# Kernel optimization log

Measured on AMD Instinct MI355X. Metric: run time of the kernel, lower is better.

## Reference

```python
import jax, jax.numpy as jnp
import numpy as np

B, H, W = 32, 512, 512

def _sample(img, sx, sy):
    """Bilinear sample img [C,H,W] at source coords sx,sy [H,W]; zeros padding (align_corners=True pixel coords)."""
    C, Hh, Ww = img.shape
    x0 = jnp.floor(sx); y0 = jnp.floor(sy)
    wx = sx - x0; wy = sy - y0
    def gat(xf, yf):
        xi = jnp.clip(xf, 0, Ww - 1).astype(jnp.int32)
        yi = jnp.clip(yf, 0, Hh - 1).astype(jnp.int32)
        valid = ((xf >= 0) & (xf <= Ww - 1) & (yf >= 0) & (yf <= Hh - 1)).astype(img.dtype)
        return img[:, yi, xi] * valid
    return (gat(x0, y0) * (1 - wx) * (1 - wy) + gat(x0 + 1, y0) * wx * (1 - wy)
            + gat(x0, y0 + 1) * (1 - wx) * wy + gat(x0 + 1, y0 + 1) * wx * wy)

def _grid(Hh, Ww, dtype):
    ys, xs = jnp.meshgrid(jnp.arange(Hh, dtype=dtype), jnp.arange(Ww, dtype=dtype), indexing='ij')
    return xs, ys

def _rotate_one(img, angle_deg):
    C, Hh, Ww = img.shape
    th = angle_deg * (jnp.pi / 180.0)
    c, s = jnp.cos(th), jnp.sin(th)
    cx, cy = (Ww - 1) / 2.0, (Hh - 1) / 2.0
    xs, ys = _grid(Hh, Ww, img.dtype)
    dx, dy = xs - cx, ys - cy
    return _sample(img, c * dx + s * dy + cx, -s * dx + c * dy + cy)

def _affine_one(img, tx, ty, sc):
    C, Hh, Ww = img.shape
    cx, cy = (Ww - 1) / 2.0, (Hh - 1) / 2.0
    xs, ys = _grid(Hh, Ww, img.dtype)
    return _sample(img, (xs - cx - tx) / sc + cx, (ys - cy - ty) / sc + cy)

def _rgb_to_hsv(img):
    r, g, b = img[:, 0], img[:, 1], img[:, 2]
    maxc = jnp.maximum(jnp.maximum(r, g), b)
    minc = jnp.minimum(jnp.minimum(r, g), b)
    delta = maxc - minc
    eps = 1e-8
    s = delta / (maxc + eps)
    dd = delta + eps
    rc, gc, bc = (maxc - r) / dd, (maxc - g) / dd, (maxc - b) / dd
    h = jnp.where(maxc == r, bc - gc, jnp.where(maxc == g, 2.0 + rc - bc, 4.0 + gc - rc))
    return (h / 6.0) % 1.0, s, maxc

def _hsv_to_rgb(h, s, v):
    i = jnp.floor(h * 6.0)
    f = h * 6.0 - i
    p, q, t = v * (1 - s), v * (1 - f * s), v * (1 - (1 - f) * s)
    i = i.astype(jnp.int32) % 6
    conds = [i == k for k in range(6)]
    r = jnp.select(conds, [v, q, p, p, t, v])
    g = jnp.select(conds, [t, v, v, q, p, p])
    b = jnp.select(conds, [p, p, t, v, v, q])
    return jnp.stack([r, g, b], axis=1)

def _color_jitter(img, bf, cf, sf, hf):
    bf, cf, sf = (x[:, None, None, None] for x in (bf, cf, sf))
    img = jnp.clip(img * bf, 0.0, 1.0)
    gray = (0.299 * img[:, 0] + 0.587 * img[:, 1] + 0.114 * img[:, 2])[:, None]
    mean = gray.mean(axis=(2, 3), keepdims=True)
    img = jnp.clip(cf * img + (1 - cf) * mean, 0.0, 1.0)
    gray = (0.299 * img[:, 0] + 0.587 * img[:, 1] + 0.114 * img[:, 2])[:, None]
    img = jnp.clip(sf * img + (1 - sf) * gray, 0.0, 1.0)
    h, s, v = _rgb_to_hsv(img)
    h = (h + hf[:, None, None]) % 1.0
    return jnp.clip(_hsv_to_rgb(h, s, v), 0.0, 1.0)

def _forward(imgs, masks, hflip_mask, vflip_mask, angles, translate, scale, brightness, contrast, saturation, hue):
    hm = (hflip_mask > 0)[:, None, None, None]
    vm = (vflip_mask > 0)[:, None, None, None]
    imgs = jnp.where(hm, imgs[..., ::-1], imgs)
    masks = jnp.where(hm, masks[..., ::-1], masks)
    imgs = jnp.where(vm, imgs[..., ::-1, :], imgs)
    masks = jnp.where(vm, masks[..., ::-1, :], masks)
    rot = jax.vmap(_rotate_one)
    imgs = rot(imgs, angles)
    masks = rot(masks, angles)
    tx = translate[:, 0] * W
    ty = translate[:, 1] * H
    aff = jax.vmap(_affine_one)
    imgs = aff(imgs, tx, ty, scale)
    masks = aff(masks, tx, ty, scale)
    imgs = _color_jitter(imgs, brightness, contrast, saturation, hue)
    return imgs, masks

def setup_inputs():
    key = jax.random.key(0)
    ks = jax.random.split(key, 11)
    return {
        "imgs": jax.random.uniform(ks[0], (B, 3, H, W), jnp.float32),
        "masks": (jax.random.uniform(ks[1], (B, 1, H, W)) > 0.5).astype(jnp.float32),
        "hflip_mask": jax.random.randint(ks[2], (B,), 0, 2, jnp.int32),
        "vflip_mask": jax.random.randint(ks[3], (B,), 0, 2, jnp.int32),
        "angles": (jax.random.uniform(ks[4], (B,)) - 0.5) * 180.0,
        "translate": (jax.random.uniform(ks[5], (B, 2)) - 0.5) * 0.2,
        "scale": 0.9 + jax.random.uniform(ks[6], (B,)) * 0.2,
        "brightness": 0.8 + jax.random.uniform(ks[7], (B,)) * 0.4,
        "contrast": 0.8 + jax.random.uniform(ks[8], (B,)) * 0.4,
        "saturation": 0.8 + jax.random.uniform(ks[9], (B,)) * 0.4,
        "hue": (jax.random.uniform(ks[10], (B,)) - 0.5) * 0.2,
    }

def reference(imgs, masks, hflip_mask, vflip_mask, angles, translate, scale, brightness, contrast, saturation, hue):
    return _forward(imgs, masks, hflip_mask, vflip_mask, angles, translate, scale, brightness, contrast, saturation, hue)
```

## Files before the change

### kernel.cpp

```cpp
#include <hip/hip_runtime.h>
#include <hip/hip_fp16.h>
#include <math.h>

#define Wd 512
#define Hd 512
#define Bd 32
#define PLANE (Hd * Wd)

#define WIN 48
#define WSTR 49

#define RPW 40
#define RPH 22

__device__ __forceinline__ float clip01(float x) { return fminf(fmaxf(x, 0.f), 1.f); }

__device__ __forceinline__ unsigned pack2h(float a, float b) {
    __half2 h = __floats2half2_rn(a, b);
    return *(unsigned*)&h;
}
__device__ __forceinline__ float2 unp2h(unsigned u) {
    return __half22float2(*(__half2*)&u);
}

__global__ __launch_bounds__(256) void k_rotate(const float* __restrict__ imgs,
                                                const float* __restrict__ masks,
                                                const int* __restrict__ hflip,
                                                const int* __restrict__ vflip,
                                                const float* __restrict__ angles,
                                                uint2* __restrict__ rot)
{
    __shared__ uint2 cells[WIN * WSTR];

    const int hw = blockIdx.x;
    const int lt = (hw & 7) * 1024 + (hw >> 3);
    const int b   = lt >> 8;
    const int t   = lt & 255;
    const int bx  = (t & 15) * 32;
    const int by  = (t >> 4) * 32;

    const int tx = threadIdx.x, ty = threadIdx.y;
    const int tid = ty * 32 + tx;

    const float cx = (Wd - 1) * 0.5f, cy = (Hd - 1) * 0.5f;
    const float th = angles[b] * 0.017453292519943295f;
    const float c = cosf(th), s = sinf(th);
    const bool hf = hflip[b] > 0, vf = vflip[b] > 0;

    const float xs0 = (float)bx - cx, xs1 = (float)(bx + 31) - cx;
    const float ys0 = (float)by - cy, ys1 = (float)(by + 31) - cy;
    float a0 = c * xs0 + s * ys0 + cx, a1 = c * xs1 + s * ys0 + cx;
    float a2 = c * xs0 + s * ys1 + cx, a3 = c * xs1 + s * ys1 + cx;
    float b0 = -s * xs0 + c * ys0 + cy, b1 = -s * xs1 + c * ys0 + cy;
    float b2 = -s * xs0 + c * ys1 + cy, b3 = -s * xs1 + c * ys1 + cy;
    float mnx = fminf(fminf(a0, a1), fminf(a2, a3));
    float mxx = fmaxf(fmaxf(a0, a1), fmaxf(a2, a3));
    float mny = fminf(fminf(b0, b1), fminf(b2, b3));
    float mxy = fmaxf(fmaxf(b0, b1), fmaxf(b2, b3));
    const int ox0 = (int)floorf(hf ? (511.f - mxx) : mnx) - 1;
    const int oy0 = (int)floorf(vf ? (511.f - mxy) : mny) - 1;

    const float* ib = imgs + (size_t)b * 3 * PLANE;
    const float* mb = masks + (size_t)b * PLANE;

    #pragma unroll
    for (int it = 0; it < 9; ++it) {
        int slot = tid + it * 256;
        int row = slot / WIN;
        int col = slot - row * WIN;
        int gi = min(max(oy0 + row, 0), Hd - 1) * Wd + min(max(ox0 + col, 0), Wd - 1);
        float r = ib[gi];
        float g = ib[gi + PLANE];
        float bl = ib[gi + 2 * PLANE];
        float m = mb[gi];
        cells[row * WSTR + col] = make_uint2(pack2h(r, g), pack2h(bl, m));
    }
    __syncthreads();

    #pragma unroll
    for (int k = 0; k < 4; ++k) {
        const int x = bx + tx, y = by + ty + k * 8;
        float dx = (float)x - cx, dy = (float)y - cy;
        float sx = c * dx + s * dy + cx;
        float sy = -s * dx + c * dy + cy;
        if (hf) sx = 511.f - sx;
        if (vf) sy = 511.f - sy;

        float sxl = sx - (float)ox0, syl = sy - (float)oy0;
        float x0f = floorf(sxl), y0f = floorf(syl);
        float wx = sxl - x0f, wy = syl - y0f;
        int xi = min(max((int)x0f, 0), WIN - 2);
        int yi = min(max((int)y0f, 0), WIN - 2);

        float fx0 = (float)ox0 + x0f, fy0 = (float)oy0 + y0f;
        float vx0 = (fx0 >= 0.f && fx0 <= 511.f) ? 1.f : 0.f;
        float vx1 = (fx0 >= -1.f && fx0 <= 510.f) ? 1.f : 0.f;
        float vy0 = (fy0 >= 0.f && fy0 <= 511.f) ? 1.f : 0.f;
        float vy1 = (fy0 >= -1.f && fy0 <= 510.f) ? 1.f : 0.f;
        float w00 = (1.f - wx) * (1.f - wy) * vx0 * vy0;
        float w10 = wx * (1.f - wy) * vx1 * vy0;
        float w01 = (1.f - wx) * wy * vx0 * vy1;
        float w11 = wx * wy * vx1 * vy1;

        int base = yi * WSTR + xi;
        uint2 c00 = cells[base],        c10 = cells[base + 1];
        uint2 c01 = cells[base + WSTR], c11 = cells[base + WSTR + 1];

        float2 rg00 = unp2h(c00.x), bm00 = unp2h(c00.y);
        float2 rg10 = unp2h(c10.x), bm10 = unp2h(c10.y);
        float2 rg01 = unp2h(c01.x), bm01 = unp2h(c01.y);
        float2 rg11 = unp2h(c11.x), bm11 = unp2h(c11.y);

        float r  = w00 * rg00.x + w10 * rg10.x + w01 * rg01.x + w11 * rg11.x;
        float g  = w00 * rg00.y + w10 * rg10.y + w01 * rg01.y + w11 * rg11.y;
        float bl = w00 * bm00.x + w10 * bm10.x + w01 * bm01.x + w11 * bm11.x;
        float m  = w00 * bm00.y + w10 * bm10.y + w01 * bm01.y + w11 * bm11.y;

        rot[(size_t)b * PLANE + (size_t)y * Wd + x] =
            make_uint2(pack2h(r, g), pack2h(bl, m));
    }
}

__global__ __launch_bounds__(256) void k_affine(const ushort4* __restrict__ rot,
                                                const float* __restrict__ translate,
                                                const float* __restrict__ scale,
                                                const float* __restrict__ brightness,
                                                unsigned short* __restrict__ pre,
                                                float* __restrict__ omasks,
                                                float* __restrict__ partials)
{
    __shared__ float4 tile[RPH * RPW];

    const int tx2 = threadIdx.x;
    const int ty  = threadIdx.y;
    const int tid = ty * 16 + tx2;
    const int bx = blockIdx.x * 32, by = blockIdx.y * 16;
    const int b = blockIdx.z;

    const float cx = (Wd - 1) * 0.5f, cy = (Hd - 1) * 0.5f;
    const float txf = translate[2 * b] * (float)Wd;
    const float tyf = translate[2 * b + 1] * (float)Hd;
    const float sc = scale[b];
    const float bf = brightness[b];

    float ax0 = ((float)bx - cx - txf) / sc + cx;
    float ax1 = ((float)(bx + 31) - cx - txf) / sc + cx;
    float ay0 = ((float)by - cy - tyf) / sc + cy;
    float ay1 = ((float)(by + 15) - cy - tyf) / sc + cy;
    const int rx0 = (int)floorf(fminf(ax0, ax1)) - 1;
    const int ry0 = (int)floorf(fminf(ay0, ay1)) - 1;

    const ushort4* srcp = rot + (size_t)b * PLANE;
    const bool fastp = (rx0 >= 0) && (ry0 >= 0) &&
                       (rx0 + RPW <= Wd) && (ry0 + RPH <= Hd);

    if (fastp) {
        for (int idx = tid; idx < RPH * RPW; idx += 256) {
            int row = idx / RPW;
            int col = idx - row * RPW;
            ushort4 h = srcp[(ry0 + row) * Wd + rx0 + col];
            tile[idx] = make_float4(__half2float(__ushort_as_half(h.x)),
                                    __half2float(__ushort_as_half(h.y)),
                                    __half2float(__ushort_as_half(h.z)),
                                    __half2float(__ushort_as_half(h.w)));
        }
    } else {
        for (int idx = tid; idx < RPH * RPW; idx += 256) {
            int row = idx / RPW;
            int col = idx - row * RPW;
            int gy = ry0 + row, gx = rx0 + col;
            float4 v = make_float4(0.f, 0.f, 0.f, 0.f);
            if ((unsigned)gy < (unsigned)Hd && (unsigned)gx < (unsigned)Wd) {
                ushort4 h = srcp[gy * Wd + gx];
                v = make_float4(__half2float(__ushort_as_half(h.x)),
                                __half2float(__ushort_as_half(h.y)),
                                __half2float(__ushort_as_half(h.z)),
                                __half2float(__ushort_as_half(h.w)));
            }
            tile[idx] = v;
        }
    }
    __syncthreads();

    float grays = 0.f;
    float rr[2], gg[2], bb[2], mm[2];
    #pragma unroll
    for (int k = 0; k < 2; ++k) {
        int x = bx + 2 * tx2 + k, y = by + ty;
        float sx = ((float)x - cx - txf) / sc + cx;
        float sy = ((float)y - cy - tyf) / sc + cy;
        float sxl = sx - (float)rx0, syl = sy - (float)ry0;
        float x0f = floorf(sxl), y0f = floorf(syl);
        float wx = sxl - x0f, wy = syl - y0f;
        int xi = min(max((int)x0f, 0), RPW - 2);
        int yi = min(max((int)y0f, 0), RPH - 2);
        float w00 = (1.f - wx) * (1.f - wy);
        float w10 = wx * (1.f - wy);
        float w01 = (1.f - wx) * wy;
        float w11 = wx * wy;
        int base = yi * RPW + xi;
        float4 v00 = tile[base], v10 = tile[base + 1];
        float4 v01 = tile[base + RPW], v11 = tile[base + RPW + 1];
        float r  = w00 * v00.x + w10 * v10.x + w01 * v01.x + w11 * v11.x;
        float g  = w00 * v00.y + w10 * v10.y + w01 * v01.y + w11 * v11.y;
        float b2 = w00 * v00.z + w10 * v10.z + w01 * v01.z + w11 * v11.z;
        float m  = w00 * v00.w + w10 * v10.w + w01 * v01.w + w11 * v11.w;
        r = clip01(r * bf);
        g = clip01(g * bf);
        b2 = clip01(b2 * bf);
        rr[k] = r; gg[k] = g; bb[k] = b2; mm[k] = m;
        grays += 0.299f * r + 0.587f * g + 0.114f * b2;
    }
    {
        size_t pix = (size_t)(by + ty) * Wd + bx + 2 * tx2;
        unsigned short* pb = pre + (size_t)b * 3 * PLANE;
        *(unsigned*)(pb + pix)             = pack2h(rr[0], rr[1]);
        *(unsigned*)(pb + PLANE + pix)     = pack2h(gg[0], gg[1]);
        *(unsigned*)(pb + 2 * PLANE + pix) = pack2h(bb[0], bb[1]);
        *(float2*)(omasks + (size_t)b * PLANE + pix) = make_float2(mm[0], mm[1]);
    }

    __syncthreads();
    float* sred = (float*)tile;
    sred[tid] = grays;
    __syncthreads();
    for (int off = 128; off > 0; off >>= 1) {
        if (tid < off) sred[tid] += sred[tid + off];
        __syncthreads();
    }
    if (tid == 0)
        partials[(size_t)b * 512 + blockIdx.y * 16 + blockIdx.x] = sred[0];
}

__global__ __launch_bounds__(256) void k_mean(const float* __restrict__ partials,
                                              float* __restrict__ means)
{
    int b = blockIdx.x;
    int t = threadIdx.x;
    float s = partials[(size_t)b * 512 + t] + partials[(size_t)b * 512 + t + 256];
    __shared__ float sr[256];
    sr[t] = s;
    __syncthreads();
    for (int off = 128; off > 0; off >>= 1) {
        if (t < off) sr[t] += sr[t + off];
        __syncthreads();
    }
    if (t == 0) means[b] = sr[0] * (1.f / (float)PLANE);
}

__device__ __forceinline__ void jit1(float& r, float& g, float& bl,
                                     float mean, float cf, float sf, float hsh)
{
    r  = clip01(cf * r + (1.f - cf) * mean);
    g  = clip01(cf * g + (1.f - cf) * mean);
    bl = clip01(cf * bl + (1.f - cf) * mean);

    float gray = 0.299f * r + 0.587f * g + 0.114f * bl;
    r  = clip01(sf * r + (1.f - sf) * gray);
    g  = clip01(sf * g + (1.f - sf) * gray);
    bl = clip01(sf * bl + (1.f - sf) * gray);

    float maxc = fmaxf(fmaxf(r, g), bl);
    float minc = fminf(fminf(r, g), bl);
    float delta = maxc - minc;
    float sgm = delta / (maxc + 1e-8f);
    float dd = delta + 1e-8f;
    float rc = (maxc - r) / dd;
    float gc = (maxc - g) / dd;
    float bc = (maxc - bl) / dd;
    float h6 = (maxc == r) ? (bc - gc) : ((maxc == g) ? (2.f + rc - bc) : (4.f + gc - rc));
    float h = h6 * (1.f / 6.f);
    h = h - floorf(h);
    h = h + hsh;
    h = h - floorf(h);

    float hi = floorf(h * 6.f);
    float f = h * 6.f - hi;
    float v = maxc;
    float p = v * (1.f - sgm);
    float q = v * (1.f - f * sgm);
    float t = v * (1.f - (1.f - f) * sgm);
    int i = ((int)hi) % 6;
    if (i < 0) i += 6;
    float ro, go, bo;
    switch (i) {
        case 0: ro = v; go = t; bo = p; break;
        case 1: ro = q; go = v; bo = p; break;
        case 2: ro = p; go = v; bo = t; break;
        case 3: ro = p; go = q; bo = v; break;
        case 4: ro = t; go = p; bo = v; break;
        default: ro = v; go = p; bo = q; break;
    }
    r = clip01(ro); g = clip01(go); bl = clip01(bo);
}

__global__ __launch_bounds__(256) void k_jitter(const unsigned short* __restrict__ pre,
                                                const float* __restrict__ means,
                                                const float* __restrict__ contrast,
                                                const float* __restrict__ saturation,
                                                const float* __restrict__ hue,
                                                float* __restrict__ oimgs)
{
    int b = blockIdx.y;
    size_t i4 = (size_t)blockIdx.x * 256 + threadIdx.x;
    const unsigned short* pb = pre + (size_t)b * 3 * PLANE;

    uint2 ur = *(const uint2*)(pb + i4 * 4);
    uint2 ug = *(const uint2*)(pb + PLANE + i4 * 4);
    uint2 ub = *(const uint2*)(pb + 2 * PLANE + i4 * 4);

    float2 r01 = unp2h(ur.x), r23 = unp2h(ur.y);
    float2 g01 = unp2h(ug.x), g23 = unp2h(ug.y);
    float2 b01 = unp2h(ub.x), b23 = unp2h(ub.y);

    float4 R  = make_float4(r01.x, r01.y, r23.x, r23.y);
    float4 G  = make_float4(g01.x, g01.y, g23.x, g23.y);
    float4 Bv = make_float4(b01.x, b01.y, b23.x, b23.y);

    float mean = means[b];
    float cf = contrast[b], sf = saturation[b], hsh = hue[b];

    jit1(R.x, G.x, Bv.x, mean, cf, sf, hsh);
    jit1(R.y, G.y, Bv.y, mean, cf, sf, hsh);
    jit1(R.z, G.z, Bv.z, mean, cf, sf, hsh);
    jit1(R.w, G.w, Bv.w, mean, cf, sf, hsh);

    size_t po = (size_t)b * 3 * PLANE + i4 * 4;
    *(float4*)(oimgs + po)             = R;
    *(float4*)(oimgs + po + PLANE)     = G;
    *(float4*)(oimgs + po + 2 * PLANE) = Bv;
}

extern "C" void kernel_launch(void* const* d_in, const int* in_sizes, int n_in,
                              void* d_out, int out_size, void* d_ws, size_t ws_size,
                              hipStream_t stream)
{
    const float* imgs       = (const float*)d_in[0];
    const float* masks      = (const float*)d_in[1];
    const int*   hflip      = (const int*)d_in[2];
    const int*   vflip      = (const int*)d_in[3];
    const float* angles     = (const float*)d_in[4];
    const float* translate  = (const float*)d_in[5];
    const float* scale      = (const float*)d_in[6];
    const float* brightness = (const float*)d_in[7];
    const float* contrast   = (const float*)d_in[8];
    const float* saturation = (const float*)d_in[9];
    const float* hue        = (const float*)d_in[10];

    float* oimgs  = (float*)d_out;
    float* omasks = oimgs + (size_t)Bd * 3 * PLANE;

    uint2* rot          = (uint2*)d_ws;
    unsigned short* pre = (unsigned short*)(rot + (size_t)Bd * PLANE);
    float* partials     = (float*)(pre + (size_t)3 * Bd * PLANE);
    float* means        = partials + (size_t)Bd * 512;

    dim3 blk1(32, 8);
    dim3 grd1(Bd * 16 * 16);
    k_rotate<<<grd1, blk1, 0, stream>>>(imgs, masks, hflip, vflip, angles, rot);

    dim3 blk2(16, 16);
    dim3 grd2(Wd / 32, Hd / 16, Bd);
    k_affine<<<grd2, blk2, 0, stream>>>((const ushort4*)rot, translate, scale, brightness,
                                        pre, omasks, partials);

    k_mean<<<Bd, 256, 0, stream>>>(partials, means);

    dim3 grd3(PLANE / 4 / 256, Bd);
    k_jitter<<<grd3, 256, 0, stream>>>(pre, means, contrast, saturation, hue, oimgs);
}
```

Measured before the change: 128.7 us.

## Vectorize halo loads, enlarge affine tiles to 32x32, keep half-precision tiles, remap blocks

The rotate kernel now aligns its halo window to even columns and loads two pixels per thread with float2 reads, writing 16-byte packed cells to shared memory. The affine kernel grows its output tile from 32x16 to 32x32 over a 40x40 window, which cuts halo overhead per output pixel. It also keeps the tile in packed half precision instead of converting to float4, which shrinks shared memory. Out-of-range samples are now zeroed through per-corner validity weights instead of a separate slow path. Blocks are remapped with a swizzled 1D grid, likely to spread them across XCDs, and the partial-sum count drops to 256 per image. The risks are more per-pixel arithmetic and possible shared-memory bank conflicts from the new strides.

```diff
diff --git a/kernel.cpp b/kernel.cpp
--- a/kernel.cpp
+++ b/kernel.cpp
@@ -8,10 +8,12 @@
 #define PLANE (Hd * Wd)
 
 #define WIN 48
-#define WSTR 49
-
-#define RPW 40
-#define RPH 22
+#define WSTR 50
+#define NPR1 (WIN * (WIN / 2))
+
+#define AWIN 40
+#define ASTR 42
+#define NPR2 (AWIN * (AWIN / 2))
 
 __device__ __forceinline__ float clip01(float x) { return fminf(fmaxf(x, 0.f), 1.f); }
 
@@ -57,23 +59,32 @@
     float mxx = fmaxf(fmaxf(a0, a1), fmaxf(a2, a3));
     float mny = fminf(fminf(b0, b1), fminf(b2, b3));
     float mxy = fmaxf(fmaxf(b0, b1), fmaxf(b2, b3));
-    const int ox0 = (int)floorf(hf ? (511.f - mxx) : mnx) - 1;
+    const int ox0 = ((int)floorf(hf ? (511.f - mxx) : mnx) - 1) & ~1;
     const int oy0 = (int)floorf(vf ? (511.f - mxy) : mny) - 1;
 
     const float* ib = imgs + (size_t)b * 3 * PLANE;
     const float* mb = masks + (size_t)b * PLANE;
 
     #pragma unroll
-    for (int it = 0; it < 9; ++it) {
+    for (int it = 0; it < 5; ++it) {
         int slot = tid + it * 256;
-        int row = slot / WIN;
-        int col = slot - row * WIN;
-        int gi = min(max(oy0 + row, 0), Hd - 1) * Wd + min(max(ox0 + col, 0), Wd - 1);
-        float r = ib[gi];
-        float g = ib[gi + PLANE];
-        float bl = ib[gi + 2 * PLANE];
-        float m = mb[gi];
-        cells[row * WSTR + col] = make_uint2(pack2h(r, g), pack2h(bl, m));
+        if (it < 4 || slot < NPR1) {
+            int row = slot / (WIN / 2);
+            int pc  = slot - row * (WIN / 2);
+            int gy = min(max(oy0 + row, 0), Hd - 1);
+            int gx = min(max(ox0 + 2 * pc, 0), Wd - 2) & ~1;
+            int gi = gy * Wd + gx;
+            float2 r2 = *(const float2*)(ib + gi);
+            float2 g2 = *(const float2*)(ib + gi + PLANE);
+            float2 b2v = *(const float2*)(ib + gi + 2 * PLANE);
+            float2 m2 = *(const float2*)(mb + gi);
+            uint4 w;
+            w.x = pack2h(r2.x, g2.x);
+            w.y = pack2h(b2v.x, m2.x);
+            w.z = pack2h(r2.y, g2.y);
+            w.w = pack2h(b2v.y, m2.y);
+            *(uint4*)&cells[row * WSTR + 2 * pc] = w;
+        }
     }
     __syncthreads();
 
@@ -121,7 +132,7 @@
     }
 }
 
-__global__ __launch_bounds__(256) void k_affine(const ushort4* __restrict__ rot,
+__global__ __launch_bounds__(256) void k_affine(const uint2* __restrict__ rot,
                                                 const float* __restrict__ translate,
                                                 const float* __restrict__ scale,
                                                 const float* __restrict__ brightness,
@@ -129,13 +140,18 @@
                                                 float* __restrict__ omasks,
                                                 float* __restrict__ partials)
 {
-    __shared__ float4 tile[RPH * RPW];
+    __shared__ uint2 tile[AWIN * ASTR];
+
+    const int hw = blockIdx.x;
+    const int lt = (hw & 7) * 1024 + (hw >> 3);
+    const int b   = lt >> 8;
+    const int t   = lt & 255;
+    const int bx  = (t & 15) * 32;
+    const int by  = (t >> 4) * 32;
 
     const int tx2 = threadIdx.x;
     const int ty  = threadIdx.y;
     const int tid = ty * 16 + tx2;
-    const int bx = blockIdx.x * 32, by = blockIdx.y * 16;
-    const int b = blockIdx.z;
 
     const float cx = (Wd - 1) * 0.5f, cy = (Hd - 1) * 0.5f;
     const float txf = translate[2 * b] * (float)Wd;
@@ -146,73 +162,72 @@
     float ax0 = ((float)bx - cx - txf) / sc + cx;
     float ax1 = ((float)(bx + 31) - cx - txf) / sc + cx;
     float ay0 = ((float)by - cy - tyf) / sc + cy;
-    float ay1 = ((float)(by + 15) - cy - tyf) / sc + cy;
-    const int rx0 = (int)floorf(fminf(ax0, ax1)) - 1;
+    float ay1 = ((float)(by + 31) - cy - tyf) / sc + cy;
+    const int rx0 = (((int)floorf(fminf(ax0, ax1)) - 1) & ~1);
     const int ry0 = (int)floorf(fminf(ay0, ay1)) - 1;
 
-    const ushort4* srcp = rot + (size_t)b * PLANE;
-    const bool fastp = (rx0 >= 0) && (ry0 >= 0) &&
-                       (rx0 + RPW <= Wd) && (ry0 + RPH <= Hd);
-
-    if (fastp) {
-        for (int idx = tid; idx < RPH * RPW; idx += 256) {
-            int row = idx / RPW;
-            int col = idx - row * RPW;
-            ushort4 h = srcp[(ry0 + row) * Wd + rx0 + col];
-            tile[idx] = make_float4(__half2float(__ushort_as_half(h.x)),
-                                    __half2float(__ushort_as_half(h.y)),
-                                    __half2float(__ushort_as_half(h.z)),
-                                    __half2float(__ushort_as_half(h.w)));
+    const uint2* sb = rot + (size_t)b * PLANE;
+
+    #pragma unroll
+    for (int it = 0; it < 4; ++it) {
+        int slot = tid + it * 256;
+        if (it < 3 || slot < NPR2) {
+            int row = slot / (AWIN / 2);
+            int pc  = slot - row * (AWIN / 2);
+            int gy = min(max(ry0 + row, 0), Hd - 1);
+            int gx = min(max(rx0 + 2 * pc, 0), Wd - 2) & ~1;
+            uint4 v = *(const uint4*)(sb + gy * Wd + gx);
+            *(uint4*)&tile[row * ASTR + 2 * pc] = v;
         }
-    } else {
-        for (int idx = tid; idx < RPH * RPW; idx += 256) {
-            int row = idx / RPW;
-            int col = idx - row * RPW;
-            int gy = ry0 + row, gx = rx0 + col;
-            float4 v = make_float4(0.f, 0.f, 0.f, 0.f);
-            if ((unsigned)gy < (unsigned)Hd && (unsigned)gx < (unsigned)Wd) {
-                ushort4 h = srcp[gy * Wd + gx];
-                v = make_float4(__half2float(__ushort_as_half(h.x)),
-                                __half2float(__ushort_as_half(h.y)),
-                                __half2float(__ushort_as_half(h.z)),
-                                __half2float(__ushort_as_half(h.w)));
-            }
-            tile[idx] = v;
+    }
+    __syncthreads();
+
+    float grays = 0.f;
+    #pragma unroll
+    for (int j = 0; j < 2; ++j) {
+        float rr[2], gg[2], bb[2], mm[2];
+        const int y = by + ty + 16 * j;
+        #pragma unroll
+        for (int k = 0; k < 2; ++k) {
+            int x = bx + 2 * tx2 + k;
+            float sx = ((float)x - cx - txf) / sc + cx;
+            float sy = ((float)y - cy - tyf) / sc + cy;
+            float sxl = sx - (float)rx0, syl = sy - (float)ry0;
+            float x0f = floorf(sxl), y0f = floorf(syl);
+            float wx = sxl - x0f, wy = syl - y0f;
+            int xi = min(max((int)x0f, 0), AWIN - 2);
+            int yi = min(max((int)y0f, 0), AWIN - 2);
+
+            float fx0 = (float)rx0 + x0f, fy0 = (float)ry0 + y0f;
+            float vx0 = (fx0 >= 0.f && fx0 <= 511.f) ? 1.f : 0.f;
+            float vx1 = (fx0 >= -1.f && fx0 <= 510.f) ? 1.f : 0.f;
+            float vy0 = (fy0 >= 0.f && fy0 <= 511.f) ? 1.f : 0.f;
+            float vy1 = (fy0 >= -1.f && fy0 <= 510.f) ? 1.f : 0.f;
+            float w00 = (1.f - wx) * (1.f - wy) * vx0 * vy0;
+            float w10 = wx * (1.f - wy) * vx1 * vy0;
+            float w01 = (1.f - wx) * wy * vx0 * vy1;
+            float w11 = wx * wy * vx1 * vy1;
+
+            int base = yi * ASTR + xi;
+            uint2 c00 = tile[base],        c10 = tile[base + 1];
+            uint2 c01 = tile[base + ASTR], c11 = tile[base + ASTR + 1];
+            float2 rg00 = unp2h(c00.x), bm00 = unp2h(c00.y);
+            float2 rg10 = unp2h(c10.x), bm10 = unp2h(c10.y);
+            float2 rg01 = unp2h(c01.x), bm01 = unp2h(c01.y);
+            float2 rg11 = unp2h(c11.x), bm11 = unp2h(c11.y);
+
+            float r  = w00 * rg00.x + w10 * rg10.x + w01 * rg01.x + w11 * rg11.x;
+            float g  = w00 * rg00.y + w10 * rg10.y + w01 * rg01.y + w11 * rg11.y;
+            float b2 = w00 * bm00.x + w10 * bm10.x + w01 * bm01.x + w11 * bm11.x;
+            float m  = w00 * bm00.y + w10 * bm10.y + w01 * bm01.y + w11 * bm11.y;
+
+            r = clip01(r * bf);
+            g = clip01(g * bf);
+            b2 = clip01(b2 * bf);
+            rr[k] = r; gg[k] = g; bb[k] = b2; mm[k] = m;
+            grays += 0.299f * r + 0.587f * g + 0.114f * b2;
         }
-    }
-    __syncthreads();
-
-    float grays = 0.f;
-    float rr[2], gg[2], bb[2], mm[2];
-    #pragma unroll
-    for (int k = 0; k < 2; ++k) {
-        int x = bx + 2 * tx2 + k, y = by + ty;
-        float sx = ((float)x - cx - txf) / sc + cx;
-        float sy = ((float)y - cy - tyf) / sc + cy;
-        float sxl = sx - (float)rx0, syl = sy - (float)ry0;
-        float x0f = floorf(sxl), y0f = floorf(syl);
-        float wx = sxl - x0f, wy = syl - y0f;
-        int xi = min(max((int)x0f, 0), RPW - 2);
-        int yi = min(max((int)y0f, 0), RPH - 2);
-        float w00 = (1.f - wx) * (1.f - wy);
-        float w10 = wx * (1.f - wy);
-        float w01 = (1.f - wx) * wy;
-        float w11 = wx * wy;
-        int base = yi * RPW + xi;
-        float4 v00 = tile[base], v10 = tile[base + 1];
-        float4 v01 = tile[base + RPW], v11 = tile[base + RPW + 1];
-        float r  = w00 * v00.x + w10 * v10.x + w01 * v01.x + w11 * v11.x;
-        float g  = w00 * v00.y + w10 * v10.y + w01 * v01.y + w11 * v11.y;
-        float b2 = w00 * v00.z + w10 * v10.z + w01 * v01.z + w11 * v11.z;
-        float m  = w00 * v00.w + w10 * v10.w + w01 * v01.w + w11 * v11.w;
-        r = clip01(r * bf);
-        g = clip01(g * bf);
-        b2 = clip01(b2 * bf);
-        rr[k] = r; gg[k] = g; bb[k] = b2; mm[k] = m;
-        grays += 0.299f * r + 0.587f * g + 0.114f * b2;
-    }
-    {
-        size_t pix = (size_t)(by + ty) * Wd + bx + 2 * tx2;
+        size_t pix = (size_t)y * Wd + bx + 2 * tx2;
         unsigned short* pb = pre + (size_t)b * 3 * PLANE;
         *(unsigned*)(pb + pix)             = pack2h(rr[0], rr[1]);
         *(unsigned*)(pb + PLANE + pix)     = pack2h(gg[0], gg[1]);
@@ -229,7 +244,7 @@
         __syncthreads();
     }
     if (tid == 0)
-        partials[(size_t)b * 512 + blockIdx.y * 16 + blockIdx.x] = sred[0];
+        partials[(size_t)b * 256 + t] = sred[0];
 }
 
 __global__ __launch_bounds__(256) void k_mean(const float* __restrict__ partials,
@@ -237,7 +252,7 @@
 {
     int b = blockIdx.x;
     int t = threadIdx.x;
-    float s = partials[(size_t)b * 512 + t] + partials[(size_t)b * 512 + t + 256];
+    float s = partials[(size_t)b * 256 + t];
     __shared__ float sr[256];
     sr[t] = s;
     __syncthreads();
@@ -353,15 +368,15 @@
     uint2* rot          = (uint2*)d_ws;
     unsigned short* pre = (unsigned short*)(rot + (size_t)Bd * PLANE);
     float* partials     = (float*)(pre + (size_t)3 * Bd * PLANE);
-    float* means        = partials + (size_t)Bd * 512;
+    float* means        = partials + (size_t)Bd * 256;
 
     dim3 blk1(32, 8);
     dim3 grd1(Bd * 16 * 16);
     k_rotate<<<grd1, blk1, 0, stream>>>(imgs, masks, hflip, vflip, angles, rot);
 
     dim3 blk2(16, 16);
-    dim3 grd2(Wd / 32, Hd / 16, Bd);
-    k_affine<<<grd2, blk2, 0, stream>>>((const ushort4*)rot, translate, scale, brightness,
+    dim3 grd2(Bd * 16 * 16);
+    k_affine<<<grd2, blk2, 0, stream>>>(rot, translate, scale, brightness,
                                         pre, omasks, partials);
 
     k_mean<<<Bd, 256, 0, stream>>>(partials, means);
```

New measurement: 118.0 us. 1.09x faster.
